# Performance work log

Hardware: AMD Instinct MI355X
Metric: run time of the kernel (lower is better)

The kernel has to match this reference:

```python
import jax, jax.numpy as jnp
import numpy as np

N = 4            # polynomial nodes per segment
SEGMENTS = 32
IN_F = 1024
OUT_F = 1024
BATCH = 32
LENGTH = 2.0
HALF = 0.5 * LENGTH
K = (N - 1) * SEGMENTS + 1  # 97 coefficients per (out,in) pair


def setup_inputs() -> dict:
    key = jax.random.key(0)
    k1, k2 = jax.random.split(key)
    x = jax.random.uniform(k1, (BATCH, IN_F), jnp.float32, -1.0, 1.0)
    wm = 1.0 / IN_F  # uniform_(-weight_magnitude/in_features, +...)
    w = jax.random.uniform(k2, (OUT_F, IN_F, K), jnp.float32, -wm, wm)
    return {"x": x, "w": w}


def _lagrange_basis(x):
    # Chebyshev-Lobatto nodes on [-1, 1]: X_k = -cos(k*pi/(n-1))
    X = -jnp.cos(jnp.arange(N) * (np.pi / (N - 1))).astype(x.dtype)
    eye = jnp.eye(N, dtype=bool)
    D = jnp.where(eye, 1.0, X[:, None] - X[None, :])      # X[j] - X[m], diag -> 1
    diff = x[..., None, None] - X                          # [..., 1, n(m)]
    ratio = jnp.where(eye, 1.0, diff / D)                  # [..., n(j), n(m)]
    return jnp.prod(ratio, axis=-1)                        # [..., n] basis_j(x)


def reference(x, w):
    # segment index per element, clamped to [0, segments-1]
    id_min = jnp.clip(((x + HALF) / LENGTH * SEGMENTS).astype(jnp.int32), 0, SEGMENTS - 1)
    id_max = id_min + 1
    wid_min = id_min * (N - 1)                             # [B, I]
    idx = wid_min[..., None] + jnp.arange(N, dtype=jnp.int32)  # [B, I, n]
    # gather per-element coefficient windows: wsel[b,i,o,j] = w[o,i,idx[b,i,j]]
    w2 = jnp.transpose(w, (1, 0, 2))                       # [I, O, K]
    wsel = jnp.take_along_axis(w2[None], idx[:, :, None, :], axis=3)  # [B, I, O, n]
    # map x into local segment coordinates on [-half, half]
    x_min = 2.0 * id_min.astype(x.dtype) / SEGMENTS - 1.0
    x_max = 2.0 * id_max.astype(x.dtype) / SEGMENTS - 1.0
    x_in = LENGTH * (x - x_min) / (x_max - x_min) - HALF   # [B, I]
    basis = _lagrange_basis(x_in)                          # [B, I, n]
    # sum over in_features and nodes: 'ijk,jkli->jl' in the original repo
    return jnp.einsum('bin,bion->bo', basis, wsel)
```

## Files before the change

### kernel.cpp

```cpp
#include <hip/hip_runtime.h>

#define IN_F   1024
#define OUT_F  1024
#define KCOEF  97
#define CROWS  32
#define CFLOATS (CROWS * KCOEF)
#define NCHUNK (IN_F / CROWS)
#define XSTRIDE 33
#define XFLOATS (CROWS * XSTRIDE)

#define ISSUE(c) do {                                                     \
    const float* _srcw = wslice + (size_t)(c) * CFLOATS;                  \
    _Pragma("unroll")                                                     \
    for (int _u = 0; _u < 12; ++_u) sw[_u] = _srcw[t + (_u << 8)];        \
    if (t < 32) sw[12] = _srcw[t + 3072];                                 \
    const int _i0 = (c) * CROWS;                                          \
    _Pragma("unroll")                                                     \
    for (int _u = 0; _u < 4; ++_u) {                                      \
        int _e = t + (_u << 8);                                           \
        sx[_u] = x[(_e >> 5) * IN_F + _i0 + (_e & 31)];                   \
    }                                                                     \
} while (0)

#define WRITE(cb_) do {                                                   \
    float* _dw = shw[cb_];                                                \
    _Pragma("unroll")                                                     \
    for (int _u = 0; _u < 12; ++_u) _dw[t + (_u << 8)] = sw[_u];          \
    if (t < 32) _dw[t + 3072] = sw[12];                                   \
    float* _dx = xs[cb_];                                                 \
    _Pragma("unroll")                                                     \
    for (int _u = 0; _u < 4; ++_u) {                                      \
        int _e = t + (_u << 8);                                           \
        _dx[(_e & 31) * XSTRIDE + (_e >> 5)] = sx[_u];                    \
    }                                                                     \
} while (0)

#define COMPUTE(cb_) do {                                                 \
    const float* _rows = &shw[cb_][(g << 2) * KCOEF];                     \
    _Pragma("unroll")                                                     \
    for (int _r = 0; _r < 4; ++_r) {                                      \
        float _xv = xs[cb_][((g << 2) + _r) * XSTRIDE + b];               \
        float _s = (_xv + 1.0f) * 16.0f;                                  \
        int _id = (int)_s;                                                \
        _id = _id < 0 ? 0 : (_id > 31 ? 31 : _id);                        \
        float _d  = _xv - ((float)_id * 0.0625f - 1.0f);                  \
        float _tt = fmaf(_d, 32.0f, -1.0f);                               \
        float _ap = _tt + 1.0f, _bp = _tt + 0.5f;                         \
        float _cm = _tt - 0.5f, _dm = _tt - 1.0f;                         \
        float _uu = _bp * _cm, _vv = _ap * _dm;                           \
        float _B0 = _uu * _dm * (-2.0f / 3.0f);                           \
        float _B1 = _vv * _cm * ( 4.0f / 3.0f);                           \
        float _B2 = _vv * _bp * (-4.0f / 3.0f);                           \
        float _B3 = _uu * _ap * ( 2.0f / 3.0f);                           \
        const float* _row = _rows + _r * KCOEF;                           \
        int _j3 = _id * 3;                                                \
        float _w0 = _row[_j3], _w1 = _row[_j3 + 1];                       \
        float _w2 = _row[_j3 + 2], _w3 = _row[_j3 + 3];                   \
        float _v = fmaf(_B0, _w0, fmaf(_B1, _w1,                          \
                   fmaf(_B2, _w2, _B3 * _w3)));                           \
        if (_r & 1) acc1 += _v; else acc0 += _v;                          \
    }                                                                     \
} while (0)

__global__ __launch_bounds__(256, 4)
void piecewise_fused(const float* __restrict__ x,
                     const float* __restrict__ w,
                     float* __restrict__ out) {
    const int bid = blockIdx.x;
    const int o = (bid & 7) * 128 + (bid >> 3);
    const int t = threadIdx.x;
    const int b = t & 31;
    const int g = t >> 5;

    __shared__ float shw[2][CFLOATS];
    __shared__ float xs[2][XFLOATS];
    __shared__ float red[256];

    const float* wslice = w + (size_t)o * (IN_F * KCOEF);

    float sw[13], sx[4];
    float acc0 = 0.f, acc1 = 0.f;

    ISSUE(0);
    WRITE(0);
    __syncthreads();

    for (int c = 0; c < NCHUNK; ++c) {
        const int cb = c & 1;
        if (c + 1 < NCHUNK) ISSUE(c + 1);
        COMPUTE(cb);
        if (c + 1 < NCHUNK) WRITE(cb ^ 1);
        __syncthreads();
    }

    red[t] = acc0 + acc1;
    __syncthreads();
    if (t < 32) {
        float sum = red[t];
        #pragma unroll
        for (int gg = 1; gg < 8; ++gg) sum += red[gg * 32 + t];
        out[t * OUT_F + o] = sum;
    }
}

extern "C" void kernel_launch(void* const* d_in, const int* in_sizes, int n_in,
                              void* d_out, int out_size, void* d_ws, size_t ws_size,
                              hipStream_t stream) {
    const float* x = (const float*)d_in[0];
    const float* w = (const float*)d_in[1];
    float*       out = (float*)d_out;
    piecewise_fused<<<OUT_F, 256, 0, stream>>>(x, w, out);
}
```

Baseline: 74.90 us.

## Give each wavefront a private slice of in-features and drop block barriers

Each of the four wavefronts now owns a contiguous quarter of the input features and double-buffers its own 8-row chunks in private shared memory, so the per-chunk __syncthreads is removed and only wave-local ordering is relied upon. A separate kernel transposes x into a workspace so each wave loads its x chunk as a coalesced float4 instead of the strided gather and padded transpose it used before. This trades block-wide barriers for an extra launch and relies on intra-wavefront lockstep for correctness of the shared-memory buffers.

```diff
diff --git a/kernel.cpp b/kernel.cpp
--- a/kernel.cpp
+++ b/kernel.cpp
@@ -3,43 +3,43 @@
 #define IN_F   1024
 #define OUT_F  1024
 #define KCOEF  97
-#define CROWS  32
-#define CFLOATS (CROWS * KCOEF)
-#define NCHUNK (IN_F / CROWS)
-#define XSTRIDE 33
-#define XFLOATS (CROWS * XSTRIDE)
+#define RPW    256
+#define RPC    8
+#define NCH    (RPW / RPC)
+#define CFL    (RPC * KCOEF)
+
+typedef float f4 __attribute__((ext_vector_type(4)));
+
+__global__ __launch_bounds__(256)
+void transpose_x(const float* __restrict__ x, float* __restrict__ xT) {
+    int t = blockIdx.x * 256 + threadIdx.x;
+    int b = t >> 10, i = t & 1023;
+    xT[(i << 5) + b] = x[t];
+}
 
 #define ISSUE(c) do {                                                     \
-    const float* _srcw = wslice + (size_t)(c) * CFLOATS;                  \
+    const float* _src = wslice + (c) * CFL;                               \
     _Pragma("unroll")                                                     \
-    for (int _u = 0; _u < 12; ++_u) sw[_u] = _srcw[t + (_u << 8)];        \
-    if (t < 32) sw[12] = _srcw[t + 3072];                                 \
-    const int _i0 = (c) * CROWS;                                          \
-    _Pragma("unroll")                                                     \
-    for (int _u = 0; _u < 4; ++_u) {                                      \
-        int _e = t + (_u << 8);                                           \
-        sx[_u] = x[(_e >> 5) * IN_F + _i0 + (_e & 31)];                   \
-    }                                                                     \
+    for (int _u = 0; _u < 12; ++_u) sw[_u] = _src[lane + (_u << 6)];      \
+    if (lane < 8) swt = _src[768 + lane];                                 \
+    sx = *(const f4*)&xslice[(c) * (RPC * 32) + (lane << 2)];             \
 } while (0)
 
 #define WRITE(cb_) do {                                                   \
-    float* _dw = shw[cb_];                                                \
+    float* _dw = shw[wv][cb_];                                            \
     _Pragma("unroll")                                                     \
-    for (int _u = 0; _u < 12; ++_u) _dw[t + (_u << 8)] = sw[_u];          \
-    if (t < 32) _dw[t + 3072] = sw[12];                                   \
-    float* _dx = xs[cb_];                                                 \
-    _Pragma("unroll")                                                     \
-    for (int _u = 0; _u < 4; ++_u) {                                      \
-        int _e = t + (_u << 8);                                           \
-        _dx[(_e & 31) * XSTRIDE + (_e >> 5)] = sx[_u];                    \
-    }                                                                     \
+    for (int _u = 0; _u < 12; ++_u) _dw[lane + (_u << 6)] = sw[_u];       \
+    if (lane < 8) _dw[768 + lane] = swt;                                  \
+    *(f4*)&shx[wv][cb_][lane << 2] = sx;                                  \
 } while (0)
 
 #define COMPUTE(cb_) do {                                                 \
-    const float* _rows = &shw[cb_][(g << 2) * KCOEF];                     \
+    const float* _rows = shw[wv][cb_];                                    \
+    const float* _xr   = shx[wv][cb_];                                    \
     _Pragma("unroll")                                                     \
-    for (int _r = 0; _r < 4; ++_r) {                                      \
-        float _xv = xs[cb_][((g << 2) + _r) * XSTRIDE + b];               \
+    for (int _r4 = 0; _r4 < 4; ++_r4) {                                   \
+        const int _r = (h << 2) + _r4;                                    \
+        float _xv = _xr[(_r << 5) + bb];                                  \
         float _s = (_xv + 1.0f) * 16.0f;                                  \
         int _id = (int)_s;                                                \
         _id = _id < 0 ? 0 : (_id > 31 ? 31 : _id);                        \
@@ -58,39 +58,41 @@
         float _w2 = _row[_j3 + 2], _w3 = _row[_j3 + 3];                   \
         float _v = fmaf(_B0, _w0, fmaf(_B1, _w1,                          \
                    fmaf(_B2, _w2, _B3 * _w3)));                           \
-        if (_r & 1) acc1 += _v; else acc0 += _v;                          \
+        if (_r4 & 1) acc1 += _v; else acc0 += _v;                         \
     }                                                                     \
 } while (0)
 
 __global__ __launch_bounds__(256, 4)
-void piecewise_fused(const float* __restrict__ x,
-                     const float* __restrict__ w,
-                     float* __restrict__ out) {
+void piecewise_main(const float* __restrict__ xT,
+                    const float* __restrict__ w,
+                    float* __restrict__ out) {
     const int bid = blockIdx.x;
     const int o = (bid & 7) * 128 + (bid >> 3);
-    const int t = threadIdx.x;
-    const int b = t & 31;
-    const int g = t >> 5;
+    const int t    = threadIdx.x;
+    const int wv   = t >> 6;
+    const int lane = t & 63;
+    const int h    = lane >> 5;
+    const int bb   = lane & 31;
 
-    __shared__ float shw[2][CFLOATS];
-    __shared__ float xs[2][XFLOATS];
+    __shared__ __align__(16) float shw[4][2][CFL];
+    __shared__ __align__(16) float shx[4][2][RPC * 32];
     __shared__ float red[256];
 
-    const float* wslice = w + (size_t)o * (IN_F * KCOEF);
+    const float* wslice = w + (size_t)o * (IN_F * KCOEF) + wv * (RPW * KCOEF);
+    const float* xslice = xT + wv * (RPW * 32);
 
-    float sw[13], sx[4];
+    float sw[12], swt;
+    f4 sx;
     float acc0 = 0.f, acc1 = 0.f;
 
     ISSUE(0);
     WRITE(0);
-    __syncthreads();
 
-    for (int c = 0; c < NCHUNK; ++c) {
+    for (int c = 0; c < NCH; ++c) {
         const int cb = c & 1;
-        if (c + 1 < NCHUNK) ISSUE(c + 1);
+        if (c + 1 < NCH) ISSUE(c + 1);
         COMPUTE(cb);
-        if (c + 1 < NCHUNK) WRITE(cb ^ 1);
-        __syncthreads();
+        if (c + 1 < NCH) WRITE(cb ^ 1);
     }
 
     red[t] = acc0 + acc1;
@@ -109,5 +111,8 @@
     const float* x = (const float*)d_in[0];
     const float* w = (const float*)d_in[1];
     float*       out = (float*)d_out;
-    piecewise_fused<<<OUT_F, 256, 0, stream>>>(x, w, out);
+    float*       xT  = (float*)d_ws;
+
+    transpose_x<<<(32 * IN_F) / 256, 256, 0, stream>>>(x, xT);
+    piecewise_main<<<OUT_F, 256, 0, stream>>>(xT, w, out);
 }
```

Measured after the change: 81.77 us. +9.2%, slower.
